# Kernel optimization log

Hardware: AMD Instinct MI355X
Metric: run time of the kernel (lower is better)

Reference implementation:

```python
import jax, jax.numpy as jnp
import numpy as np
from jax import lax

KH, KW = 3, 3
K = KH * KW
STRIDE, PAD, DIL = 1, 1, 1
CIN, COUT = 64, 64


def setup_inputs() -> dict:
    key = jax.random.key(0)
    k1, k2, k3, k4 = jax.random.split(key, 4)
    B, H, W = 8, 96, 96
    x = jax.random.normal(k1, (B, CIN, H, W), dtype=jnp.float32)
    # offset/mask conv params (small so sampled offsets stay near the grid)
    w_off = jax.random.normal(k2, (3 * K, CIN, KH, KW), dtype=jnp.float32) * 0.01
    b_off = jnp.zeros((3 * K,), dtype=jnp.float32)
    # main deformable conv weight, uniform(-stdv, stdv) like reset_parameters
    stdv = 1.0 / np.sqrt(CIN * KH * KW)
    weight = jax.random.uniform(k3, (COUT, CIN, KH, KW), dtype=jnp.float32,
                                minval=-stdv, maxval=stdv)
    bias = jax.random.normal(k4, (COUT,), dtype=jnp.float32) * 0.01
    return {"x": x, "w_off": w_off, "b_off": b_off, "weight": weight, "bias": bias}


def _bilinear_sample(img, ys, xs):
    # img: [C,H,W]; ys, xs: [K,Ho,Wo] float sample coords. Zero outside borders.
    C, H, W = img.shape
    y0 = jnp.floor(ys)
    x0 = jnp.floor(xs)
    wy1 = ys - y0  # weight for y0+1
    wx1 = xs - x0
    wy0 = 1.0 - wy1
    wx0 = 1.0 - wx1

    def gather(yi, xi):
        yc = jnp.clip(yi, 0, H - 1).astype(jnp.int32)
        xc = jnp.clip(xi, 0, W - 1).astype(jnp.int32)
        valid = ((yi >= 0) & (yi <= H - 1) & (xi >= 0) & (xi <= W - 1))
        # [C,K,Ho,Wo]
        return img[:, yc, xc] * valid.astype(img.dtype)[None]

    return (gather(y0, x0) * (wy0 * wx0)[None]
            + gather(y0, x0 + 1) * (wy0 * wx1)[None]
            + gather(y0 + 1, x0) * (wy1 * wx0)[None]
            + gather(y0 + 1, x0 + 1) * (wy1 * wx1)[None])


def reference(x, w_off, b_off, weight, bias):
    B, C, H, W = x.shape
    # offset/mask conv (same geometry as main conv)
    om = lax.conv_general_dilated(
        x, w_off, window_strides=(STRIDE, STRIDE),
        padding=[(PAD, PAD), (PAD, PAD)], rhs_dilation=(DIL, DIL),
        dimension_numbers=("NCHW", "OIHW", "NCHW")) + b_off[None, :, None, None]
    Ho, Wo = om.shape[2], om.shape[3]
    offset = om[:, :2 * K].reshape(B, K, 2, Ho, Wo)  # interleaved (dy,dx) per tap
    dy, dx = offset[:, :, 0], offset[:, :, 1]         # [B,K,Ho,Wo]
    mask = jax.nn.sigmoid(om[:, 2 * K:])              # [B,K,Ho,Wo]

    k = jnp.arange(K)
    ky = (k // KW).astype(jnp.float32) * DIL  # [K]
    kx = (k % KW).astype(jnp.float32) * DIL
    oy = jnp.arange(Ho, dtype=jnp.float32) * STRIDE - PAD  # [Ho]
    ox = jnp.arange(Wo, dtype=jnp.float32) * STRIDE - PAD  # [Wo]
    ys = oy[None, None, :, None] + ky[None, :, None, None] + dy  # [B,K,Ho,Wo]
    xs = ox[None, None, None, :] + kx[None, :, None, None] + dx

    sampled = jax.vmap(_bilinear_sample)(x, ys, xs)  # [B,C,K,Ho,Wo]
    w_r = weight.reshape(weight.shape[0], C, K)      # [O,C,K]
    out = jnp.einsum("bkhw,bckhw,ock->bohw", mask, sampled, w_r)
    return out + bias[None, :, None, None]
```

## Files before the change

kernel.cpp:

```cpp
#include <hip/hip_runtime.h>
#include <math.h>

typedef __bf16 b16x8 __attribute__((ext_vector_type(8)));
typedef float  f32x4 __attribute__((ext_vector_type(4)));

#define B_    8
#define CIN_  64
#define COUT_ 64
#define Hs    96
#define Ws    96
#define PLANE (Hs*Ws)
#define IMG   (CIN_*PLANE)
#define NP    (B_*PLANE)
#define NBLK  (NP/32)

#define WR 8
#define WC 24
#define WPIX (WR*WC)
#define WBYTES (WPIX*128)

__device__ __forceinline__ int swz(int bid) { return (bid & 7) * (NBLK / 8) + (bid >> 3); }

__global__ void prep_xpose(const float* __restrict__ x,
                           const float* __restrict__ weight, const float* __restrict__ w_off,
                           __bf16* __restrict__ xT,
                           __bf16* __restrict__ wAB, __bf16* __restrict__ wAO) {
    int bid = blockIdx.x;
    if (bid < 288) {
        int p = bid * 256 + threadIdx.x;
        int b = p / PLANE, r = p - b * PLANE;
        const float* src = x + b * IMG + r;
        __bf16 buf[64];
#pragma unroll
        for (int c = 0; c < 64; ++c) buf[c] = (__bf16)src[c * PLANE];
        b16x8* dst = (b16x8*)(xT + (size_t)p * 64);
#pragma unroll
        for (int j = 0; j < 8; ++j) dst[j] = ((const b16x8*)buf)[j];
    } else {
        int i = (bid - 288) * 256 + threadIdx.x;
        if (i < 36864) {
            int e = i & 7, lane = (i >> 3) & 63, mt = (i >> 9) & 3, ks = (i >> 11) & 1, k = i >> 12;
            int o = mt * 16 + (lane & 15);
            int c = ks * 32 + ((lane >> 4) << 3) + e;
            wAB[i] = (__bf16)weight[o * 576 + c * 9 + k];
        }
        if (i < 18432) {
            int e = i & 7, lane = (i >> 3) & 63, mt = (i >> 9) & 1, ks = (i >> 10) & 1, t = i >> 11;
            int ch = mt * 16 + (lane & 15);
            int c  = ks * 32 + ((lane >> 4) << 3) + e;
            wAO[i] = (ch < 27) ? (__bf16)w_off[ch * 576 + c * 9 + t] : (__bf16)(0.f);
        }
    }
}

__global__ __launch_bounds__(256, 4)
void deform_mfma(const __bf16* __restrict__ xT,
                 const __bf16* __restrict__ wAO,
                 const float* __restrict__ b_off,
                 const __bf16* __restrict__ wAB,
                 const float* __restrict__ bias,
                 float* __restrict__ out) {
    __shared__ __align__(16) unsigned char smemWin[WBYTES];
    __shared__ float omP[2][2][28][16];

    int tid  = threadIdx.x;
    int lane = tid & 63;
    int g    = __builtin_amdgcn_readfirstlane(tid >> 6);
    int s    = g & 1;
    int kh   = g >> 1;
    int n    = lane & 15;
    int q    = lane >> 4;

    int t    = swz(blockIdx.x);
    int b    = t / 288;
    int rem  = t - b * 288;
    int rp   = rem / 6;
    int ct   = rem - rp * 6;
    int h0   = rp * 2;
    int c0   = ct * 16;
    int hrow = h0 + s;
    int w    = c0 + n;

    const __bf16* xTimg = xT + (size_t)b * PLANE * 64;
    const __bf16* xTb   = xTimg + kh * 32 + q * 8;

    const b16x8* wAOv = (const b16x8*)wAO;
    const b16x8* wABv = (const b16x8*)wAB;
    int boff = kh * 64 + q * 16;

#define LDSRD(sl) (*(const b16x8*)(smemWin + (sl) * 128 + (boff ^ (((sl) & 7) << 4))))

#pragma unroll
    for (int r2 = 0; r2 < 6; ++r2) {
        int idx = tid + r2 * 256;
        int pix = idx >> 3, j = idx & 7;
        int yw = pix / WC, xw = pix - yw * WC;
        int ys = min(max(h0 - 3 + yw, 0), Hs - 1);
        int xs = min(max(c0 - 3 + xw, 0), Ws - 1);
        b16x8 v = *(const b16x8*)(xTimg + ((ys * Ws + xs) * 64) + j * 8);
        *(b16x8*)(smemWin + pix * 128 + ((j * 16) ^ ((pix & 7) << 4))) = v;
    }
    __syncthreads();

    f32x4 accA0 = {0.f, 0.f, 0.f, 0.f};
    f32x4 accA1 = {0.f, 0.f, 0.f, 0.f};
    const b16x8 ZER = {};

#pragma unroll 3
    for (int tt = 0; tt < 9; ++tt) {
        int ky = tt / 3, kx = tt - ky * 3;
        int yy = hrow - 1 + ky, xx = w - 1 + kx;
        bool mk = (yy >= 0 && yy < Hs && xx >= 0 && xx < Ws);
        int sl = (s + 2 + ky) * WC + (n + 2 + kx);
        b16x8 bf = LDSRD(sl);
        bf = mk ? bf : ZER;
        b16x8 af0 = wAOv[((tt * 2 + kh) * 2 + 0) * 64 + lane];
        b16x8 af1 = wAOv[((tt * 2 + kh) * 2 + 1) * 64 + lane];
        accA0 = __builtin_amdgcn_mfma_f32_16x16x32_bf16(af0, bf, accA0, 0, 0, 0);
        accA1 = __builtin_amdgcn_mfma_f32_16x16x32_bf16(af1, bf, accA1, 0, 0, 0);
    }
#pragma unroll
    for (int rg = 0; rg < 4; ++rg) {
        int ch = q * 4 + rg;
        omP[s][kh][ch][n] = accA0[rg] + (kh ? 0.f : b_off[ch]);
    }
#pragma unroll
    for (int rg = 0; rg < 4; ++rg) {
        int ch = 16 + q * 4 + rg;
        if (ch < 27) omP[s][kh][ch][n] = accA1[rg] + (kh ? 0.f : b_off[ch]);
    }
    __syncthreads();

    f32x4 acc0 = {0.f, 0.f, 0.f, 0.f};
    f32x4 acc1 = {0.f, 0.f, 0.f, 0.f};
    f32x4 acc2 = {0.f, 0.f, 0.f, 0.f};
    f32x4 acc3 = {0.f, 0.f, 0.f, 0.f};

    const float* om0 = &omP[s][0][0][0];
    const float* om1 = &omP[s][1][0][0];

#pragma unroll 3
    for (int k = 0; k < 9; ++k) {
        float dy = om0[(2 * k) * 16 + n]     + om1[(2 * k) * 16 + n];
        float dx = om0[(2 * k + 1) * 16 + n] + om1[(2 * k + 1) * 16 + n];
        float mo = om0[(18 + k) * 16 + n]    + om1[(18 + k) * 16 + n];

        b16x8 a0 = wABv[(k * 8 + kh * 4 + 0) * 64 + lane];
        b16x8 a1 = wABv[(k * 8 + kh * 4 + 1) * 64 + lane];
        b16x8 a2 = wABv[(k * 8 + kh * 4 + 2) * 64 + lane];
        b16x8 a3 = wABv[(k * 8 + kh * 4 + 3) * 64 + lane];

        float m  = 1.f / (1.f + __expf(-mo));
        int ky = k / 3, kx = k - ky * 3;
        float ysf = (float)(hrow - 1 + ky) + dy;
        float xsf = (float)(w    - 1 + kx) + dx;
        float y0f = floorf(ysf), x0f = floorf(xsf);
        float ly = ysf - y0f, lx = xsf - x0f;
        float hy = 1.f - ly, hx = 1.f - lx;
        int y0 = (int)y0f, x0 = (int)x0f, y1 = y0 + 1, x1 = x0 + 1;
        bool vy0 = (y0 >= 0) && (y0 < Hs), vy1 = (y1 >= 0) && (y1 < Hs);
        bool vx0 = (x0 >= 0) && (x0 < Ws), vx1 = (x1 >= 0) && (x1 < Ws);
        float W00 = (vy0 && vx0) ? m * hy * hx : 0.f;
        float W01 = (vy0 && vx1) ? m * hy * lx : 0.f;
        float W10 = (vy1 && vx0) ? m * ly * hx : 0.f;
        float W11 = (vy1 && vx1) ? m * ly * lx : 0.f;

        bool inw = (y0 >= h0 - 3) && (y1 <= h0 + 4) && (x0 >= c0 - 3) && (x1 <= c0 + 20);

        b16x8 e00, e01, e10, e11;
        if (inw) {
            int sl = (y0 - (h0 - 3)) * WC + (x0 - (c0 - 3));
            e00 = LDSRD(sl);
            e01 = LDSRD(sl + 1);
            e10 = LDSRD(sl + WC);
            e11 = LDSRD(sl + WC + 1);
        } else {
            int y0c = min(max(y0, 0), Hs - 1), y1c = min(max(y1, 0), Hs - 1);
            int x0c = min(max(x0, 0), Ws - 1), x1c = min(max(x1, 0), Ws - 1);
            e00 = *(const b16x8*)(xTb + (y0c * Ws + x0c) * 64);
            e01 = *(const b16x8*)(xTb + (y0c * Ws + x1c) * 64);
            e10 = *(const b16x8*)(xTb + (y1c * Ws + x0c) * 64);
            e11 = *(const b16x8*)(xTb + (y1c * Ws + x1c) * 64);
        }

        b16x8 fe;
#pragma unroll
        for (int j = 0; j < 8; ++j)
            fe[j] = (__bf16)((float)e00[j] * W00 + (float)e01[j] * W01 +
                             (float)e10[j] * W10 + (float)e11[j] * W11);

        acc0 = __builtin_amdgcn_mfma_f32_16x16x32_bf16(a0, fe, acc0, 0, 0, 0);
        acc1 = __builtin_amdgcn_mfma_f32_16x16x32_bf16(a1, fe, acc1, 0, 0, 0);
        acc2 = __builtin_amdgcn_mfma_f32_16x16x32_bf16(a2, fe, acc2, 0, 0, 0);
        acc3 = __builtin_amdgcn_mfma_f32_16x16x32_bf16(a3, fe, acc3, 0, 0, 0);
    }
#undef LDSRD

    __syncthreads();
    float* xch = (float*)smemWin;
    {
        f32x4* xw = (f32x4*)&xch[((s * 2 + kh) * 64 + lane) * 8];
        if (kh == 0) { xw[0] = acc2; xw[1] = acc3; }
        else         { xw[0] = acc0; xw[1] = acc1; }
    }
    __syncthreads();
    {
        const f32x4* xr = (const f32x4*)&xch[((s * 2 + (kh ^ 1)) * 64 + lane) * 8];
        f32x4 t0 = xr[0], t1 = xr[1];
        int rr = hrow * Ws + w;
        int ob = b * (COUT_ * PLANE) + rr;
        if (kh == 0) {
            f32x4 bs0 = *(const f32x4*)&bias[q * 4];
            f32x4 bs1 = *(const f32x4*)&bias[16 + q * 4];
#pragma unroll
            for (int rg = 0; rg < 4; ++rg) { int o =      q * 4 + rg; out[ob + o * PLANE] = acc0[rg] + t0[rg] + bs0[rg]; }
#pragma unroll
            for (int rg = 0; rg < 4; ++rg) { int o = 16 + q * 4 + rg; out[ob + o * PLANE] = acc1[rg] + t1[rg] + bs1[rg]; }
        } else {
            f32x4 bs2 = *(const f32x4*)&bias[32 + q * 4];
            f32x4 bs3 = *(const f32x4*)&bias[48 + q * 4];
#pragma unroll
            for (int rg = 0; rg < 4; ++rg) { int o = 32 + q * 4 + rg; out[ob + o * PLANE] = acc2[rg] + t0[rg] + bs2[rg]; }
#pragma unroll
            for (int rg = 0; rg < 4; ++rg) { int o = 48 + q * 4 + rg; out[ob + o * PLANE] = acc3[rg] + t1[rg] + bs3[rg]; }
        }
    }
}

extern "C" void kernel_launch(void* const* d_in, const int* in_sizes, int n_in,
                              void* d_out, int out_size, void* d_ws, size_t ws_size,
                              hipStream_t stream) {
    const float* x      = (const float*)d_in[0];
    const float* w_off  = (const float*)d_in[1];
    const float* b_off  = (const float*)d_in[2];
    const float* weight = (const float*)d_in[3];
    const float* bias   = (const float*)d_in[4];
    float* out = (float*)d_out;

    char* ws = (char*)d_ws;
    __bf16* wAB = (__bf16*)ws;
    __bf16* wAO = (__bf16*)(ws + 73728);
    __bf16* xT  = (__bf16*)(ws + 131072);

    prep_xpose<<<432, 256, 0, stream>>>(x, weight, w_off, xT, wAB, wAO);
    deform_mfma<<<NBLK, 256, 0, stream>>>(xT, wAO, b_off, wAB, bias, out);
}
```

Before: 115.1 us.

## Give each wave a full output row with all channels, doubling block tile height

Each block now covers 4 output rows by 16 columns, and each wave handles one row across all 64 input channels. Before, two waves split the channel halves of the same row. This drops the cross-wave partial-sum exchange through LDS, the extra barriers, and the duplicated per-pixel offset, mask and bilinear-weight math. The shared window grows to 10 rows, so halo reloads per output pixel go down. The cost is twice the per-wave register and MFMA work and half as many blocks, which could raise register pressure under the existing launch bounds.

```diff
diff --git a/kernel.cpp b/kernel.cpp
--- a/kernel.cpp
+++ b/kernel.cpp
@@ -12,9 +12,9 @@
 #define PLANE (Hs*Ws)
 #define IMG   (CIN_*PLANE)
 #define NP    (B_*PLANE)
-#define NBLK  (NP/32)
-
-#define WR 8
+#define NBLK  (NP/64)
+
+#define WR 10
 #define WC 24
 #define WPIX (WR*WC)
 #define WBYTES (WPIX*128)
@@ -61,44 +61,44 @@
                  const float* __restrict__ bias,
                  float* __restrict__ out) {
     __shared__ __align__(16) unsigned char smemWin[WBYTES];
-    __shared__ float omP[2][2][28][16];
+    __shared__ float omL[4][27 * 16];
 
     int tid  = threadIdx.x;
     int lane = tid & 63;
-    int g    = __builtin_amdgcn_readfirstlane(tid >> 6);
-    int s    = g & 1;
-    int kh   = g >> 1;
+    int s    = __builtin_amdgcn_readfirstlane(tid >> 6);
     int n    = lane & 15;
     int q    = lane >> 4;
 
     int t    = swz(blockIdx.x);
-    int b    = t / 288;
-    int rem  = t - b * 288;
-    int rp   = rem / 6;
-    int ct   = rem - rp * 6;
-    int h0   = rp * 2;
+    int b    = t / 144;
+    int rem  = t - b * 144;
+    int rq   = rem / 6;
+    int ct   = rem - rq * 6;
+    int h0   = rq * 4;
     int c0   = ct * 16;
     int hrow = h0 + s;
     int w    = c0 + n;
 
     const __bf16* xTimg = xT + (size_t)b * PLANE * 64;
-    const __bf16* xTb   = xTimg + kh * 32 + q * 8;
+    const __bf16* xTb   = xTimg + q * 8;
 
     const b16x8* wAOv = (const b16x8*)wAO;
     const b16x8* wABv = (const b16x8*)wAB;
-    int boff = kh * 64 + q * 16;
-
-#define LDSRD(sl) (*(const b16x8*)(smemWin + (sl) * 128 + (boff ^ (((sl) & 7) << 4))))
-
-#pragma unroll
-    for (int r2 = 0; r2 < 6; ++r2) {
+    int boff = q * 16;
+
+#define LDSRD(sl, off) (*(const b16x8*)(smemWin + (sl) * 128 + ((off) ^ (((sl) & 7) << 4))))
+
+#pragma unroll
+    for (int r2 = 0; r2 < 8; ++r2) {
         int idx = tid + r2 * 256;
-        int pix = idx >> 3, j = idx & 7;
-        int yw = pix / WC, xw = pix - yw * WC;
-        int ys = min(max(h0 - 3 + yw, 0), Hs - 1);
-        int xs = min(max(c0 - 3 + xw, 0), Ws - 1);
-        b16x8 v = *(const b16x8*)(xTimg + ((ys * Ws + xs) * 64) + j * 8);
-        *(b16x8*)(smemWin + pix * 128 + ((j * 16) ^ ((pix & 7) << 4))) = v;
+        if (r2 < 7 || tid < (WPIX * 8 - 1792)) {
+            int pix = idx >> 3, j = idx & 7;
+            int yw = pix / WC, xw = pix - yw * WC;
+            int ys = min(max(h0 - 3 + yw, 0), Hs - 1);
+            int xs = min(max(c0 - 3 + xw, 0), Ws - 1);
+            b16x8 v = *(const b16x8*)(xTimg + ((ys * Ws + xs) * 64) + j * 8);
+            *(b16x8*)(smemWin + pix * 128 + ((j * 16) ^ ((pix & 7) << 4))) = v;
+        }
     }
     __syncthreads();
 
@@ -112,43 +112,35 @@
         int yy = hrow - 1 + ky, xx = w - 1 + kx;
         bool mk = (yy >= 0 && yy < Hs && xx >= 0 && xx < Ws);
         int sl = (s + 2 + ky) * WC + (n + 2 + kx);
-        b16x8 bf = LDSRD(sl);
-        bf = mk ? bf : ZER;
-        b16x8 af0 = wAOv[((tt * 2 + kh) * 2 + 0) * 64 + lane];
-        b16x8 af1 = wAOv[((tt * 2 + kh) * 2 + 1) * 64 + lane];
-        accA0 = __builtin_amdgcn_mfma_f32_16x16x32_bf16(af0, bf, accA0, 0, 0, 0);
-        accA1 = __builtin_amdgcn_mfma_f32_16x16x32_bf16(af1, bf, accA1, 0, 0, 0);
-    }
-#pragma unroll
-    for (int rg = 0; rg < 4; ++rg) {
-        int ch = q * 4 + rg;
-        omP[s][kh][ch][n] = accA0[rg] + (kh ? 0.f : b_off[ch]);
-    }
-#pragma unroll
-    for (int rg = 0; rg < 4; ++rg) {
-        int ch = 16 + q * 4 + rg;
-        if (ch < 27) omP[s][kh][ch][n] = accA1[rg] + (kh ? 0.f : b_off[ch]);
-    }
-    __syncthreads();
+        b16x8 bf0 = LDSRD(sl, boff);
+        b16x8 bf1 = LDSRD(sl, boff + 64);
+        bf0 = mk ? bf0 : ZER;
+        bf1 = mk ? bf1 : ZER;
+        b16x8 af0 = wAOv[((tt * 2 + 0) * 2 + 0) * 64 + lane];
+        b16x8 af1 = wAOv[((tt * 2 + 0) * 2 + 1) * 64 + lane];
+        b16x8 af2 = wAOv[((tt * 2 + 1) * 2 + 0) * 64 + lane];
+        b16x8 af3 = wAOv[((tt * 2 + 1) * 2 + 1) * 64 + lane];
+        accA0 = __builtin_amdgcn_mfma_f32_16x16x32_bf16(af0, bf0, accA0, 0, 0, 0);
+        accA1 = __builtin_amdgcn_mfma_f32_16x16x32_bf16(af1, bf0, accA1, 0, 0, 0);
+        accA0 = __builtin_amdgcn_mfma_f32_16x16x32_bf16(af2, bf1, accA0, 0, 0, 0);
+        accA1 = __builtin_amdgcn_mfma_f32_16x16x32_bf16(af3, bf1, accA1, 0, 0, 0);
+    }
+    float* omW = &omL[s][0];
+#pragma unroll
+    for (int rg = 0; rg < 4; ++rg) { int ch = q * 4 + rg;      omW[ch * 16 + n] = accA0[rg] + b_off[ch]; }
+#pragma unroll
+    for (int rg = 0; rg < 4; ++rg) { int ch = 16 + q * 4 + rg; if (ch < 27) omW[ch * 16 + n] = accA1[rg] + b_off[ch]; }
 
     f32x4 acc0 = {0.f, 0.f, 0.f, 0.f};
     f32x4 acc1 = {0.f, 0.f, 0.f, 0.f};
     f32x4 acc2 = {0.f, 0.f, 0.f, 0.f};
     f32x4 acc3 = {0.f, 0.f, 0.f, 0.f};
 
-    const float* om0 = &omP[s][0][0][0];
-    const float* om1 = &omP[s][1][0][0];
-
 #pragma unroll 3
     for (int k = 0; k < 9; ++k) {
-        float dy = om0[(2 * k) * 16 + n]     + om1[(2 * k) * 16 + n];
-        float dx = om0[(2 * k + 1) * 16 + n] + om1[(2 * k + 1) * 16 + n];
-        float mo = om0[(18 + k) * 16 + n]    + om1[(18 + k) * 16 + n];
-
-        b16x8 a0 = wABv[(k * 8 + kh * 4 + 0) * 64 + lane];
-        b16x8 a1 = wABv[(k * 8 + kh * 4 + 1) * 64 + lane];
-        b16x8 a2 = wABv[(k * 8 + kh * 4 + 2) * 64 + lane];
-        b16x8 a3 = wABv[(k * 8 + kh * 4 + 3) * 64 + lane];
+        float dy = omW[(2 * k) * 16 + n];
+        float dx = omW[(2 * k + 1) * 16 + n];
+        float mo = omW[(18 + k) * 16 + n];
 
         float m  = 1.f / (1.f + __expf(-mo));
         int ky = k / 3, kx = k - ky * 3;
@@ -165,66 +157,73 @@
         float W10 = (vy1 && vx0) ? m * ly * hx : 0.f;
         float W11 = (vy1 && vx1) ? m * ly * lx : 0.f;
 
-        bool inw = (y0 >= h0 - 3) && (y1 <= h0 + 4) && (x0 >= c0 - 3) && (x1 <= c0 + 20);
-
-        b16x8 e00, e01, e10, e11;
+        bool inw = (y0 >= h0 - 3) && (y1 <= h0 + 6) && (x0 >= c0 - 3) && (x1 <= c0 + 20);
+
+        b16x8 e00, e01, e10, e11, o00, o01, o10, o11;
         if (inw) {
             int sl = (y0 - (h0 - 3)) * WC + (x0 - (c0 - 3));
-            e00 = LDSRD(sl);
-            e01 = LDSRD(sl + 1);
-            e10 = LDSRD(sl + WC);
-            e11 = LDSRD(sl + WC + 1);
+            e00 = LDSRD(sl, boff);           o00 = LDSRD(sl, boff + 64);
+            e01 = LDSRD(sl + 1, boff);       o01 = LDSRD(sl + 1, boff + 64);
+            e10 = LDSRD(sl + WC, boff);      o10 = LDSRD(sl + WC, boff + 64);
+            e11 = LDSRD(sl + WC + 1, boff);  o11 = LDSRD(sl + WC + 1, boff + 64);
         } else {
             int y0c = min(max(y0, 0), Hs - 1), y1c = min(max(y1, 0), Hs - 1);
             int x0c = min(max(x0, 0), Ws - 1), x1c = min(max(x1, 0), Ws - 1);
-            e00 = *(const b16x8*)(xTb + (y0c * Ws + x0c) * 64);
-            e01 = *(const b16x8*)(xTb + (y0c * Ws + x1c) * 64);
-            e10 = *(const b16x8*)(xTb + (y1c * Ws + x0c) * 64);
-            e11 = *(const b16x8*)(xTb + (y1c * Ws + x1c) * 64);
-        }
+            const b16x8* P00 = (const b16x8*)(xTb + (y0c * Ws + x0c) * 64);
+            const b16x8* P01 = (const b16x8*)(xTb + (y0c * Ws + x1c) * 64);
+            const b16x8* P10 = (const b16x8*)(xTb + (y1c * Ws + x0c) * 64);
+            const b16x8* P11 = (const b16x8*)(xTb + (y1c * Ws + x1c) * 64);
+            e00 = P00[0]; o00 = P00[4];
+            e01 = P01[0]; o01 = P01[4];
+            e10 = P10[0]; o10 = P10[4];
+            e11 = P11[0]; o11 = P11[4];
+        }
+
+        b16x8 a0 = wABv[(k * 8 + 0) * 64 + lane];
+        b16x8 a1 = wABv[(k * 8 + 1) * 64 + lane];
+        b16x8 a2 = wABv[(k * 8 + 2) * 64 + lane];
+        b16x8 a3 = wABv[(k * 8 + 3) * 64 + lane];
 
         b16x8 fe;
 #pragma unroll
         for (int j = 0; j < 8; ++j)
             fe[j] = (__bf16)((float)e00[j] * W00 + (float)e01[j] * W01 +
                              (float)e10[j] * W10 + (float)e11[j] * W11);
-
         acc0 = __builtin_amdgcn_mfma_f32_16x16x32_bf16(a0, fe, acc0, 0, 0, 0);
         acc1 = __builtin_amdgcn_mfma_f32_16x16x32_bf16(a1, fe, acc1, 0, 0, 0);
         acc2 = __builtin_amdgcn_mfma_f32_16x16x32_bf16(a2, fe, acc2, 0, 0, 0);
         acc3 = __builtin_amdgcn_mfma_f32_16x16x32_bf16(a3, fe, acc3, 0, 0, 0);
+
+        b16x8 a4 = wABv[(k * 8 + 4) * 64 + lane];
+        b16x8 a5 = wABv[(k * 8 + 5) * 64 + lane];
+        b16x8 a6 = wABv[(k * 8 + 6) * 64 + lane];
+        b16x8 a7 = wABv[(k * 8 + 7) * 64 + lane];
+
+        b16x8 fo;
+#pragma unroll
+        for (int j = 0; j < 8; ++j)
+            fo[j] = (__bf16)((float)o00[j] * W00 + (float)o01[j] * W01 +
+                             (float)o10[j] * W10 + (float)o11[j] * W11);
+        acc0 = __builtin_amdgcn_mfma_f32_16x16x32_bf16(a4, fo, acc0, 0, 0, 0);
+        acc1 = __builtin_amdgcn_mfma_f32_16x16x32_bf16(a5, fo, acc1, 0, 0, 0);
+        acc2 = __builtin_amdgcn_mfma_f32_16x16x32_bf16(a6, fo, acc2, 0, 0, 0);
+        acc3 = __builtin_amdgcn_mfma_f32_16x16x32_bf16(a7, fo, acc3, 0, 0, 0);
     }
 #undef LDSRD
 
-    __syncthreads();
-    float* xch = (float*)smemWin;
-    {
-        f32x4* xw = (f32x4*)&xch[((s * 2 + kh) * 64 + lane) * 8];
-        if (kh == 0) { xw[0] = acc2; xw[1] = acc3; }
-        else         { xw[0] = acc0; xw[1] = acc1; }
-    }
-    __syncthreads();
-    {
-        const f32x4* xr = (const f32x4*)&xch[((s * 2 + (kh ^ 1)) * 64 + lane) * 8];
-        f32x4 t0 = xr[0], t1 = xr[1];
-        int rr = hrow * Ws + w;
-        int ob = b * (COUT_ * PLANE) + rr;
-        if (kh == 0) {
-            f32x4 bs0 = *(const f32x4*)&bias[q * 4];
-            f32x4 bs1 = *(const f32x4*)&bias[16 + q * 4];
-#pragma unroll
-            for (int rg = 0; rg < 4; ++rg) { int o =      q * 4 + rg; out[ob + o * PLANE] = acc0[rg] + t0[rg] + bs0[rg]; }
-#pragma unroll
-            for (int rg = 0; rg < 4; ++rg) { int o = 16 + q * 4 + rg; out[ob + o * PLANE] = acc1[rg] + t1[rg] + bs1[rg]; }
-        } else {
-            f32x4 bs2 = *(const f32x4*)&bias[32 + q * 4];
-            f32x4 bs3 = *(const f32x4*)&bias[48 + q * 4];
-#pragma unroll
-            for (int rg = 0; rg < 4; ++rg) { int o = 32 + q * 4 + rg; out[ob + o * PLANE] = acc2[rg] + t0[rg] + bs2[rg]; }
-#pragma unroll
-            for (int rg = 0; rg < 4; ++rg) { int o = 48 + q * 4 + rg; out[ob + o * PLANE] = acc3[rg] + t1[rg] + bs3[rg]; }
-        }
-    }
+    int ob = b * (COUT_ * PLANE) + hrow * Ws + w;
+    f32x4 bs0 = *(const f32x4*)&bias[q * 4];
+    f32x4 bs1 = *(const f32x4*)&bias[16 + q * 4];
+    f32x4 bs2 = *(const f32x4*)&bias[32 + q * 4];
+    f32x4 bs3 = *(const f32x4*)&bias[48 + q * 4];
+#pragma unroll
+    for (int rg = 0; rg < 4; ++rg) { int o =      q * 4 + rg; out[ob + o * PLANE] = acc0[rg] + bs0[rg]; }
+#pragma unroll
+    for (int rg = 0; rg < 4; ++rg) { int o = 16 + q * 4 + rg; out[ob + o * PLANE] = acc1[rg] + bs1[rg]; }
+#pragma unroll
+    for (int rg = 0; rg < 4; ++rg) { int o = 32 + q * 4 + rg; out[ob + o * PLANE] = acc2[rg] + bs2[rg]; }
+#pragma unroll
+    for (int rg = 0; rg < 4; ++rg) { int o = 48 + q * 4 + rg; out[ob + o * PLANE] = acc3[rg] + bs3[rg]; }
 }
 
 extern "C" void kernel_launch(void* const* d_in, const int* in_sizes, int n_in,
```

Measured after the change: 117.9 us. +2.5%, slower.
